# Optimization experiments

Hardware: AMD Instinct MI355X
Metric: run time of the kernel (lower is better)

Reference implementation:

```python
import jax, jax.numpy as jnp
import numpy as np

D = 8       # path dimension (inferred: siglen = sum_{k=1..M} D**k)
M = 6       # signature truncation level
BATCH = 128
SIGLEN = sum(D**k for k in range(1, M + 1))  # 299592


def setup_inputs() -> dict:
    key = jax.random.key(0)
    k1, k2 = jax.random.split(key)
    x = jax.random.normal(k1, (BATCH, SIGLEN), dtype=jnp.float32)
    y = jax.random.normal(k2, (BATCH, D), dtype=jnp.float32)
    return {"x": x, "y": y}


def _sigjoin(x, y, d, m):
    """Chen's identity: sig(path * linear_segment(y)) = x (tensor-prod) exp(y),
    truncated at level m. x is the flattened signature (levels 1..m),
    y is the displacement of the appended linear segment."""
    b = x.shape[0]
    sizes = [d ** k for k in range(1, m + 1)]
    offs = np.cumsum([0] + sizes)
    # split flat signature into per-level tensors: x_lvl[k-1] has shape (b, d**k)
    x_lvl = [x[:, offs[i]:offs[i + 1]] for i in range(m)]
    # truncated tensor exponential of the linear segment: e_k = y^{\otimes k} / k!
    e_lvl = [y]
    for k in range(2, m + 1):
        e = jnp.einsum('bi,bj->bij', e_lvl[-1], y).reshape(b, -1) / k
        e_lvl.append(e)
    # Chen product, level k: z_k = x_k + e_k + sum_{i=1}^{k-1} x_i (outer) e_{k-i}
    out = []
    for k in range(1, m + 1):
        z = x_lvl[k - 1] + e_lvl[k - 1]
        for i in range(1, k):
            z = z + jnp.einsum('bi,bj->bij', x_lvl[i - 1], e_lvl[k - i - 1]).reshape(b, -1)
        out.append(z)
    return jnp.concatenate(out, axis=-1)


def reference(x, y):
    return _sigjoin(x, y, D, M)
```

## Files before the change

### kernel.cpp

```cpp
#include <hip/hip_runtime.h>


#define SIGLEN 299592

__global__ __launch_bounds__(256) void sigjoin_kernel(
    const float* __restrict__ x, const float* __restrict__ y,
    float* __restrict__ out)
{
    __shared__ float sy[8];
    __shared__ float sf[8];
    const int row = blockIdx.y;
    if (threadIdx.x < 8) {
        sy[threadIdx.x] = y[row * 8 + threadIdx.x];
        const float f[8] = {1.f, 1.f, 0.5f, 1.f/6.f, 1.f/24.f,
                            1.f/120.f, 1.f/720.f, 1.f/5040.f};
        sf[threadIdx.x] = f[threadIdx.x];
    }
    __syncthreads();

    const int g   = blockIdx.x * blockDim.x + threadIdx.x;
    const int col = g * 4;
    if (col >= SIGLEN) return;

    const float* __restrict__ xrow = x   + (size_t)row * SIGLEN;
    float* __restrict__       orow = out + (size_t)row * SIGLEN;

    int k, loff;
    if      (col >= 37448) { k = 6; loff = 37448; }
    else if (col >=  4680) { k = 5; loff =  4680; }
    else if (col >=   584) { k = 4; loff =   584; }
    else if (col >=    72) { k = 3; loff =    72; }
    else if (col >=     8) { k = 2; loff =     8; }
    else                   { k = 1; loff =     0; }

    const int j  = col - loff;
    const int d0 = j & 7;
    int tt = j >> 3;

    float S = 0.f;
    float Q = 1.f;
    int   O = (loff >> 3) - 1;
    for (int i = k - 1; i >= 1; --i) {
        S += xrow[O + tt] * Q * sf[k - i];
        Q *= sy[tt & 7];
        tt >>= 3;
        O = (O >> 3) - 1;
    }
    S += Q * sf[k];

    const float4 xv = *(const float4*)(xrow + col);
    float4 zv;
    zv.x = xv.x + S * sy[d0 + 0];
    zv.y = xv.y + S * sy[d0 + 1];
    zv.z = xv.z + S * sy[d0 + 2];
    zv.w = xv.w + S * sy[d0 + 3];
    *(float4*)(orow + col) = zv;
}

extern "C" void kernel_launch(void* const* d_in, const int* in_sizes, int n_in,
                              void* d_out, int out_size, void* d_ws, size_t ws_size,
                              hipStream_t stream) {
    const float* x = (const float*)d_in[0];
    const float* y = (const float*)d_in[1];
    float* out = (float*)d_out;

    const int groups = SIGLEN / 4;
    const int bx = (groups + 255) / 256;
    dim3 grid(bx, 128, 1);
    dim3 block(256, 1, 1);
    hipLaunchKernelGGL(sigjoin_kernel, grid, block, 0, stream, x, y, out);
}
```

Baseline: 288.0 us.

## Share level-6 Horner prefix in shared memory across each block's tile

Level-6 blocks now handle aligned 1024-element tiles. Each tile's common lower-level prefix (G3, G4, G5) is built once per block through shared memory and three staged barriers, instead of every thread redoing a 5-step Horner loop with scattered gathers from x. Lower levels keep the per-thread path in a separate set of blocks. This cuts redundant global reads and ALU work for the dominant level, at the cost of extra __syncthreads and idle threads during the staged prefix computation.

New measurement: 268.7 us. 6.7% less time.

```diff
diff --git a/kernel.cpp b/kernel.cpp
--- a/kernel.cpp
+++ b/kernel.cpp
@@ -2,6 +2,8 @@
 
 
 #define SIGLEN 299592
+#define L6_OFF 37448
+#define NAIVE_BLOCKS 37
 
 __global__ __launch_bounds__(256) void sigjoin_kernel(
     const float* __restrict__ x, const float* __restrict__ y,
@@ -9,52 +11,97 @@
 {
     __shared__ float sy[8];
     __shared__ float sf[8];
+    __shared__ float sG3[2];
+    __shared__ float sG4[16];
+    __shared__ float sG5[128];
+
     const int row = blockIdx.y;
-    if (threadIdx.x < 8) {
-        sy[threadIdx.x] = y[row * 8 + threadIdx.x];
+    const int tid = threadIdx.x;
+    if (tid < 8) {
+        sy[tid] = y[row * 8 + tid];
         const float f[8] = {1.f, 1.f, 0.5f, 1.f/6.f, 1.f/24.f,
                             1.f/120.f, 1.f/720.f, 1.f/5040.f};
-        sf[threadIdx.x] = f[threadIdx.x];
+        sf[tid] = f[tid];
     }
     __syncthreads();
-
-    const int g   = blockIdx.x * blockDim.x + threadIdx.x;
-    const int col = g * 4;
-    if (col >= SIGLEN) return;
 
     const float* __restrict__ xrow = x   + (size_t)row * SIGLEN;
     float* __restrict__       orow = out + (size_t)row * SIGLEN;
 
-    int k, loff;
-    if      (col >= 37448) { k = 6; loff = 37448; }
-    else if (col >=  4680) { k = 5; loff =  4680; }
-    else if (col >=   584) { k = 4; loff =   584; }
-    else if (col >=    72) { k = 3; loff =    72; }
-    else if (col >=     8) { k = 2; loff =     8; }
-    else                   { k = 1; loff =     0; }
+    if (blockIdx.x >= NAIVE_BLOCKS) {
+        const int base6 = (blockIdx.x - NAIVE_BLOCKS) * 1024;
 
-    const int j  = col - loff;
-    const int d0 = j & 7;
-    int tt = j >> 3;
+        if (tid == 0) {
+            const int p  = base6 >> 15;
+            const int w  = base6 >> 12;
+            const int v0 = base6 >> 9;
+            const float x1v = xrow[p];
+            const float x2v = xrow[8 + w];
+            const float x3a = xrow[72 + v0];
+            const float x3b = xrow[72 + v0 + 1];
+            const float G0 = 1.f / 720.f;
+            const float G1 = x1v * (1.f/120.f) + sy[p & 7] * G0;
+            const float G2 = x2v * (1.f/24.f)  + sy[w & 7] * G1;
+            sG3[0] = x3a * (1.f/6.f) + sy[v0 & 7] * G2;
+            sG3[1] = x3b * (1.f/6.f) + sy[(v0 + 1) & 7] * G2;
+        }
+        __syncthreads();
+        if (tid < 16) {
+            const int u0 = base6 >> 6;
+            sG4[tid] = xrow[584 + u0 + tid] * 0.5f + sy[tid & 7] * sG3[tid >> 3];
+        }
+        __syncthreads();
+        if (tid < 128) {
+            const int t0 = base6 >> 3;
+            sG5[tid] = xrow[4680 + t0 + tid] + sy[tid & 7] * sG4[tid >> 3];
+        }
+        __syncthreads();
 
-    float S = 0.f;
-    float Q = 1.f;
-    int   O = (loff >> 3) - 1;
-    for (int i = k - 1; i >= 1; --i) {
-        S += xrow[O + tt] * Q * sf[k - i];
-        Q *= sy[tt & 7];
-        tt >>= 3;
-        O = (O >> 3) - 1;
+        const int j  = base6 + tid * 4;
+        const float S = sG5[tid >> 1];
+        const int d0 = (tid & 1) * 4;
+        const float4 xv = *(const float4*)(xrow + L6_OFF + j);
+        float4 zv;
+        zv.x = xv.x + S * sy[d0 + 0];
+        zv.y = xv.y + S * sy[d0 + 1];
+        zv.z = xv.z + S * sy[d0 + 2];
+        zv.w = xv.w + S * sy[d0 + 3];
+        *(float4*)(orow + L6_OFF + j) = zv;
+    } else {
+        const int g   = blockIdx.x * 256 + tid;
+        const int col = g * 4;
+        if (col >= L6_OFF) return;
+
+        int k, loff;
+        if      (col >= 4680) { k = 5; loff = 4680; }
+        else if (col >=  584) { k = 4; loff =  584; }
+        else if (col >=   72) { k = 3; loff =   72; }
+        else if (col >=    8) { k = 2; loff =    8; }
+        else                  { k = 1; loff =    0; }
+
+        const int j  = col - loff;
+        const int d0 = j & 7;
+        int tt = j >> 3;
+
+        float S = 0.f;
+        float Q = 1.f;
+        int   O = (loff >> 3) - 1;
+        for (int i = k - 1; i >= 1; --i) {
+            S += xrow[O + tt] * Q * sf[k - i];
+            Q *= sy[tt & 7];
+            tt >>= 3;
+            O = (O >> 3) - 1;
+        }
+        S += Q * sf[k];
+
+        const float4 xv = *(const float4*)(xrow + col);
+        float4 zv;
+        zv.x = xv.x + S * sy[d0 + 0];
+        zv.y = xv.y + S * sy[d0 + 1];
+        zv.z = xv.z + S * sy[d0 + 2];
+        zv.w = xv.w + S * sy[d0 + 3];
+        *(float4*)(orow + col) = zv;
     }
-    S += Q * sf[k];
-
-    const float4 xv = *(const float4*)(xrow + col);
-    float4 zv;
-    zv.x = xv.x + S * sy[d0 + 0];
-    zv.y = xv.y + S * sy[d0 + 1];
-    zv.z = xv.z + S * sy[d0 + 2];
-    zv.w = xv.w + S * sy[d0 + 3];
-    *(float4*)(orow + col) = zv;
 }
 
 extern "C" void kernel_launch(void* const* d_in, const int* in_sizes, int n_in,
@@ -64,9 +111,7 @@
     const float* y = (const float*)d_in[1];
     float* out = (float*)d_out;
 
-    const int groups = SIGLEN / 4;
-    const int bx = (groups + 255) / 256;
-    dim3 grid(bx, 128, 1);
+    dim3 grid(NAIVE_BLOCKS + 256, 128, 1);
     dim3 block(256, 1, 1);
     hipLaunchKernelGGL(sigjoin_kernel, grid, block, 0, stream, x, y, out);
 }
```
